# Optimization experiments

Hardware: AMD Instinct MI355X
Metric: run time of the kernel (lower is better)

## Reference

```python
import jax, jax.numpy as jnp
import numpy as np

N = 100000   # nodes
E = 1600000  # edges
IN = 32      # input_dim == num_concepts
H = 128      # h_dim == num_concepts * dim_per_concept
C = 32       # num_concepts
D = 4        # dim_per_concept
G = 32       # g_dim of per-concept MLPs
LAMBDAV = 1e-3


def _spmm(edge_src, edge_dst, edge_val, x):
    # sparse adjacency matmul: out[d] = sum_{edges e: dst(e)=d} val(e) * x[src(e)]
    return jax.ops.segment_sum(edge_val[:, None] * x[edge_src], edge_dst, num_segments=N)


def setup_inputs() -> dict:
    key = jax.random.key(0)
    ks = jax.random.split(key, 20)
    s = lambda shape: 1.0 / np.sqrt(shape[-1] if len(shape) > 1 else 1)
    inp = {
        'X': jax.random.normal(ks[0], (N, IN), jnp.float32),
        'label': jax.random.uniform(ks[1], (N, C), jnp.float32),
        'edge_val': jax.random.uniform(ks[2], (E,), jnp.float32),
        'noise': jax.random.normal(ks[3], (N, C, D), jnp.float32),
        'W_base': jax.random.normal(ks[4], (IN, H), jnp.float32) / np.sqrt(IN),
        'W_mean': jax.random.normal(ks[5], (H, H), jnp.float32) / np.sqrt(H),
        'W_logstd': jax.random.normal(ks[6], (H, H), jnp.float32) / np.sqrt(H),
        'A': 0.05 * jax.random.normal(ks[7], (C, C), jnp.float32),  # keep I - A^T well-conditioned
        'Wz1': jax.random.normal(ks[8], (C, D, G), jnp.float32) / np.sqrt(D),
        'bz1': jax.random.normal(ks[9], (C, G), jnp.float32) * 0.01,
        'Wz2': jax.random.normal(ks[10], (C, G, D), jnp.float32) / np.sqrt(G),
        'bz2': jax.random.normal(ks[11], (C, D), jnp.float32) * 0.01,
        'Wl1': jax.random.normal(ks[12], (C, 1, G), jnp.float32),
        'bl1': jax.random.normal(ks[13], (C, G), jnp.float32) * 0.01,
        'Wl2': jax.random.normal(ks[14], (C, G, 1), jnp.float32) / np.sqrt(G),
        'bl2': jax.random.normal(ks[15], (C, 1), jnp.float32) * 0.01,
        'Wrec': jax.random.normal(ks[16], (H, IN), jnp.float32) / np.sqrt(H),
        'brec': jax.random.normal(ks[17], (IN,), jnp.float32) * 0.01,
        'edge_src': jax.random.randint(ks[18], (E,), 0, N),
        'edge_dst': jax.random.randint(ks[19], (E,), 0, N),
    }
    return inp


def reference(X, label, edge_val, noise, W_base, W_mean, W_logstd, A,
              Wz1, bz1, Wz2, bz2, Wl1, bl1, Wl2, bl2, Wrec, brec,
              edge_src, edge_dst):
    # ---- sparse GCN encoder (x branch): GraphConvSparse = act(spmm(adj, x @ W)) ----
    hidden = jax.nn.relu(_spmm(edge_src, edge_dst, edge_val, X @ W_base))   # [N, H]
    e_m = _spmm(edge_src, edge_dst, edge_val, hidden @ W_mean)              # [N, H]
    _ = _spmm(edge_src, edge_dst, edge_val, hidden @ W_logstd)              # computed then discarded (e_v := ones) in source
    e_m = e_m.reshape(N, C, D)                                              # [N, C, D]

    # ---- CausalDAG: z = (I - A^T)^{-1} epsilon along the concept axis ----
    I = jnp.eye(C, dtype=X.dtype)
    Cmat = jnp.linalg.inv(I - A.T)                                          # [C, C]
    z_m = jnp.einsum('ck,nkd->ncd', Cmat, e_m)                              # [N, C, D]

    # mask: A^T @ x along concept axis
    masked_z_m = jnp.einsum('ck,nkd->ncd', A.T, z_m)                        # [N, C, D]
    masked_label = jnp.einsum('ck,nk->nc', A.T, label)[..., None]           # [N, C, 1]

    # g_z: per-concept MLP Linear(D,G)-ELU-Linear(G,D), weights stacked over concepts
    hz = jax.nn.elu(jnp.einsum('ncd,cdg->ncg', masked_z_m, Wz1) + bz1[None])
    masked_z_m = jnp.einsum('ncg,cgd->ncd', hz, Wz2) + bz2[None]            # [N, C, D]

    # g_label: per-concept MLP Linear(1,G)-ELU-Linear(G,1)
    hl = jax.nn.elu(jnp.einsum('nce,ceg->ncg', masked_label, Wl1) + bl1[None])
    pred_label = (jnp.einsum('ncg,cge->nce', hl, Wl2) + bl2[None])[..., 0]  # [N, C]

    # conditional_sample_gaussian with v = e_v * lambdav, e_v = ones
    z = masked_z_m + jnp.sqrt(jnp.asarray(LAMBDAV, X.dtype)) * noise        # [N, C, D]

    # pred_x / reconst_X head
    rec_x = z.reshape(N, H) @ Wrec + brec                                   # [N, IN]
    return rec_x, pred_label
```

## Files before the change

kernel.cpp:

```cpp
#include <hip/hip_runtime.h>
#include <hip/hip_bf16.h>

#define N_NODES 100000
#define N_EDGES 1600000
#define NBUCK   391

static __device__ __forceinline__ float us2f(unsigned short u) {
    union { unsigned int i; float f; } cv; cv.i = ((unsigned int)u) << 16; return cv.f;
}
static __device__ __forceinline__ unsigned short f2us(float f) {
    __hip_bfloat16 b = __float2bfloat16(f);
    union { __hip_bfloat16 b; unsigned short u; } cv; cv.b = b; return cv.u;
}
static __device__ __forceinline__ float elu_fast(float v) {
    return v > 0.f ? v : (__expf(v) - 1.0f);
}

__global__ __launch_bounds__(64) void k_inv(const float* __restrict__ A,
                                            float* __restrict__ MmT) {
    __shared__ float Af[1024];
    __shared__ float aug[32 * 65];
    __shared__ float fac[32];
    __shared__ float pv_s;
    int t = threadIdx.x;
    for (int i = t; i < 1024; i += 64) Af[i] = A[i];
    __syncthreads();
    for (int i = t; i < 2048; i += 64) {
        int r = i >> 6, c = i & 63;
        float v;
        if (c < 32) v = (r == c ? 1.0f : 0.0f) - Af[c * 32 + r];
        else        v = ((c - 32) == r ? 1.0f : 0.0f);
        aug[r * 65 + c] = v;
    }
    __syncthreads();
    for (int k = 0; k < 32; ++k) {
        if (t == 0) pv_s = 1.0f / aug[k * 65 + k];
        __syncthreads();
        aug[k * 65 + t] *= pv_s;
        __syncthreads();
        if (t < 32) fac[t] = aug[t * 65 + k];
        __syncthreads();
        #pragma unroll 4
        for (int i = t; i < 2048; i += 64) {
            int r = i >> 6, c = i & 63;
            if (r != k) aug[r * 65 + c] -= fac[r] * aug[k * 65 + c];
        }
        __syncthreads();
    }
    for (int i = t; i < 1024; i += 64) {
        int j = i >> 5, c = i & 31;
        float s = 0.f;
        #pragma unroll
        for (int k = 0; k < 32; ++k) s += Af[k * 32 + c] * aug[k * 65 + 32 + j];
        MmT[i] = s;
    }
}

__global__ __launch_bounds__(256) void k_fold(const float* __restrict__ MmT,
                                              const float* __restrict__ Wm,
                                              float* __restrict__ Wcomb) {
    __shared__ float MmTs[1024];
    int tid = threadIdx.x;
    for (int i = tid; i < 1024; i += 256) MmTs[i] = MmT[i];
    __syncthreads();
    int o = blockIdx.x * 256 + tid;
    int h = o >> 5, c = o & 31;
    float4 s = {0.f, 0.f, 0.f, 0.f};
    #pragma unroll
    for (int j = 0; j < 32; ++j) {
        float m = MmTs[j * 32 + c];
        float4 w = ((const float4*)Wm)[h * 32 + j];
        s.x += m * w.x; s.y += m * w.y; s.z += m * w.z; s.w += m * w.w;
    }
    ((float4*)Wcomb)[o] = s;
}

__global__ __launch_bounds__(256) void k_hist(const int* __restrict__ edst,
                                              unsigned int* __restrict__ deg) {
    int e = blockIdx.x * 256 + threadIdx.x;
    atomicAdd(&deg[edst[e]], 1u);
}

__global__ __launch_bounds__(256) void k_scanA(const unsigned int* __restrict__ deg,
                                               unsigned int* __restrict__ row_start,
                                               unsigned int* __restrict__ blk_sums) {
    __shared__ unsigned int sums[256];
    int tid = threadIdx.x;
    int gid = blockIdx.x * 256 + tid;
    uint4 d = ((const uint4*)deg)[gid];
    unsigned int p1 = d.x, p2 = d.x + d.y, p3 = p2 + d.z;
    unsigned int tsum = p3 + d.w;
    sums[tid] = tsum;
    __syncthreads();
    for (int off = 1; off < 256; off <<= 1) {
        unsigned int v = (tid >= off) ? sums[tid - off] : 0u;
        __syncthreads();
        sums[tid] += v;
        __syncthreads();
    }
    unsigned int excl = sums[tid] - tsum;
    int eb = gid * 4;
    if (eb + 0 < N_NODES) row_start[eb + 0] = excl;
    if (eb + 1 < N_NODES) row_start[eb + 1] = excl + p1;
    if (eb + 2 < N_NODES) row_start[eb + 2] = excl + p2;
    if (eb + 3 < N_NODES) row_start[eb + 3] = excl + p3;
    if (tid == 255) blk_sums[blockIdx.x] = sums[255];
}

__global__ __launch_bounds__(128) void k_scanB(unsigned int* __restrict__ blk_sums) {
    __shared__ unsigned int s[128];
    int tid = threadIdx.x;
    unsigned int v = (tid < 98) ? blk_sums[tid] : 0u;
    s[tid] = v;
    __syncthreads();
    for (int off = 1; off < 128; off <<= 1) {
        unsigned int x = (tid >= off) ? s[tid - off] : 0u;
        __syncthreads();
        s[tid] += x;
        __syncthreads();
    }
    if (tid < 98) blk_sums[tid] = s[tid] - v;
}

__global__ __launch_bounds__(256) void k_scanC(unsigned int* __restrict__ row_start,
                                               unsigned int* __restrict__ cursor,
                                               const unsigned int* __restrict__ blk_sums) {
    int tid = threadIdx.x;
    unsigned int off = blk_sums[blockIdx.x];
    int eb = (blockIdx.x * 256 + tid) * 4;
    #pragma unroll
    for (int k = 0; k < 4; ++k) {
        int idx = eb + k;
        if (idx < N_NODES) {
            unsigned int u = row_start[idx] + off;
            row_start[idx] = u;
            cursor[idx] = u;
        }
    }
    if (blockIdx.x == 0 && tid == 0) row_start[N_NODES] = N_EDGES;
}

__global__ __launch_bounds__(256) void k_binit(const unsigned int* __restrict__ row_start,
                                               unsigned int* __restrict__ bucket_cursor) {
    int b = blockIdx.x * 256 + threadIdx.x;
    if (b < NBUCK) bucket_cursor[b] = row_start[b << 8];
}

__global__ __launch_bounds__(256) void k_bucket1(const int* __restrict__ esrc,
                                                 const int* __restrict__ edst,
                                                 const float* __restrict__ evalv,
                                                 unsigned int* __restrict__ bucket_cursor,
                                                 uint2* __restrict__ coarse,
                                                 unsigned char* __restrict__ coarse_dl) {
    __shared__ unsigned int hist[NBUCK];
    __shared__ unsigned int gbase[NBUCK];
    __shared__ unsigned int lcnt[NBUCK];
    int tid = threadIdx.x;
    int e0 = blockIdx.x * 8192;
    for (int i = tid; i < NBUCK; i += 256) { hist[i] = 0u; lcnt[i] = 0u; }
    __syncthreads();
    #pragma unroll 4
    for (int k = 0; k < 32; ++k) {
        int e = e0 + k * 256 + tid;
        if (e < N_EDGES) atomicAdd(&hist[((unsigned)edst[e]) >> 8], 1u);
    }
    __syncthreads();
    for (int b = tid; b < NBUCK; b += 256) {
        unsigned int h = hist[b];
        gbase[b] = h ? atomicAdd(&bucket_cursor[b], h) : 0u;
    }
    __syncthreads();
    #pragma unroll 4
    for (int k = 0; k < 32; ++k) {
        int e = e0 + k * 256 + tid;
        if (e < N_EDGES) {
            unsigned int d = (unsigned)edst[e];
            unsigned int b = d >> 8;
            unsigned int r = atomicAdd(&lcnt[b], 1u);
            unsigned int p = gbase[b] + r;
            uint2 ev;
            ev.x = (unsigned int)esrc[e];
            ev.y = __float_as_uint(evalv[e]);
            coarse[p] = ev;
            coarse_dl[p] = (unsigned char)(d & 255u);
        }
    }
}

__global__ __launch_bounds__(256) void k_bucket2(const unsigned int* __restrict__ row_start,
                                                 const uint2* __restrict__ coarse,
                                                 const unsigned char* __restrict__ coarse_dl,
                                                 unsigned int* __restrict__ cursor,
                                                 uint2* __restrict__ edge_sorted) {
    int b = blockIdx.x;
    unsigned int bs = row_start[b << 8];
    unsigned int be = (b == NBUCK - 1) ? N_EDGES : row_start[(b + 1) << 8];
    unsigned int nbase = (unsigned)b << 8;
    for (unsigned int i = bs + threadIdx.x; i < be; i += 256) {
        uint2 ev = coarse[i];
        unsigned int d = nbase | (unsigned int)coarse_dl[i];
        unsigned int p = atomicAdd(&cursor[d], 1u);
        edge_sorted[p] = ev;
    }
}

__global__ __launch_bounds__(256) void k_gather1(const unsigned int* __restrict__ row_start,
                                                 const uint2* __restrict__ edge_sorted,
                                                 const float* __restrict__ X,
                                                 float* __restrict__ S1) {
    int lane = threadIdx.x & 31;
    int n = blockIdx.x * 8 + (threadIdx.x >> 5);
    unsigned int i = row_start[n], e = row_start[n + 1];
    float a0 = 0.f, a1 = 0.f, a2 = 0.f, a3 = 0.f;
    for (; i + 4 <= e; i += 4) {
        uint2 ea = edge_sorted[i + 0], eb = edge_sorted[i + 1];
        uint2 ec = edge_sorted[i + 2], ed = edge_sorted[i + 3];
        float xa = X[(size_t)ea.x * 32 + lane];
        float xb = X[(size_t)eb.x * 32 + lane];
        float xc = X[(size_t)ec.x * 32 + lane];
        float xd = X[(size_t)ed.x * 32 + lane];
        a0 += __uint_as_float(ea.y) * xa;
        a1 += __uint_as_float(eb.y) * xb;
        a2 += __uint_as_float(ec.y) * xc;
        a3 += __uint_as_float(ed.y) * xd;
    }
    for (; i < e; ++i) {
        uint2 ea = edge_sorted[i];
        a0 += __uint_as_float(ea.y) * X[(size_t)ea.x * 32 + lane];
    }
    S1[(size_t)n * 32 + lane] = (a0 + a1) + (a2 + a3);
}

__global__ __launch_bounds__(256) void k_gemm1(const float* __restrict__ S1,
                                               const float* __restrict__ Wb,
                                               unsigned short* __restrict__ hidden) {
    __shared__ float Wb_s[4096];
    __shared__ float S1s[32 * 36];
    int tid = threadIdx.x;
    int n0 = blockIdx.x * 32;
    for (int i = tid; i < 1024; i += 256)
        ((float4*)Wb_s)[i] = ((const float4*)Wb)[i];
    {
        int r = tid >> 3, cq = tid & 7;
        *(float4*)&S1s[r * 36 + cq * 4] = *(const float4*)&S1[(size_t)(n0 + r) * 32 + cq * 4];
    }
    __syncthreads();
    int q = (tid & 31) * 4;
    int r0 = tid >> 5;
    float4 acc[4];
    #pragma unroll
    for (int i = 0; i < 4; ++i) acc[i] = make_float4(0.f, 0.f, 0.f, 0.f);
    for (int k4 = 0; k4 < 32; k4 += 4) {
        float4 s[4];
        #pragma unroll
        for (int i = 0; i < 4; ++i) s[i] = *(const float4*)&S1s[(r0 + i * 8) * 36 + k4];
        #pragma unroll
        for (int kk = 0; kk < 4; ++kk) {
            float4 w = *(const float4*)&Wb_s[(k4 + kk) * 128 + q];
            #pragma unroll
            for (int i = 0; i < 4; ++i) {
                float v = (&s[i].x)[kk];
                acc[i].x += v * w.x; acc[i].y += v * w.y;
                acc[i].z += v * w.z; acc[i].w += v * w.w;
            }
        }
    }
    #pragma unroll
    for (int i = 0; i < 4; ++i) {
        ushort4 o;
        o.x = f2us(fmaxf(acc[i].x, 0.f)); o.y = f2us(fmaxf(acc[i].y, 0.f));
        o.z = f2us(fmaxf(acc[i].z, 0.f)); o.w = f2us(fmaxf(acc[i].w, 0.f));
        *(ushort4*)&hidden[(size_t)(n0 + r0 + i * 8) * 128 + q] = o;
    }
}

__global__ __launch_bounds__(256) void k_gather2(const unsigned int* __restrict__ row_start,
                                                 const uint2* __restrict__ edge_sorted,
                                                 const unsigned short* __restrict__ hidden,
                                                 unsigned short* __restrict__ S2) {
    int lane = threadIdx.x & 31;
    int n = blockIdx.x * 8 + (threadIdx.x >> 5);
    unsigned int i = row_start[n], e = row_start[n + 1];
    float4 A0 = {0, 0, 0, 0}, A1 = {0, 0, 0, 0}, A2 = {0, 0, 0, 0}, A3 = {0, 0, 0, 0};
    for (; i + 4 <= e; i += 4) {
        uint2 ea = edge_sorted[i + 0], eb = edge_sorted[i + 1];
        uint2 ec = edge_sorted[i + 2], ed = edge_sorted[i + 3];
        ushort4 ha = *(const ushort4*)&hidden[(size_t)ea.x * 128 + lane * 4];
        ushort4 hb = *(const ushort4*)&hidden[(size_t)eb.x * 128 + lane * 4];
        ushort4 hc = *(const ushort4*)&hidden[(size_t)ec.x * 128 + lane * 4];
        ushort4 hd = *(const ushort4*)&hidden[(size_t)ed.x * 128 + lane * 4];
        float va = __uint_as_float(ea.y), vb = __uint_as_float(eb.y);
        float vc = __uint_as_float(ec.y), vd = __uint_as_float(ed.y);
        A0.x += va * us2f(ha.x); A0.y += va * us2f(ha.y); A0.z += va * us2f(ha.z); A0.w += va * us2f(ha.w);
        A1.x += vb * us2f(hb.x); A1.y += vb * us2f(hb.y); A1.z += vb * us2f(hb.z); A1.w += vb * us2f(hb.w);
        A2.x += vc * us2f(hc.x); A2.y += vc * us2f(hc.y); A2.z += vc * us2f(hc.z); A2.w += vc * us2f(hc.w);
        A3.x += vd * us2f(hd.x); A3.y += vd * us2f(hd.y); A3.z += vd * us2f(hd.z); A3.w += vd * us2f(hd.w);
    }
    for (; i < e; ++i) {
        uint2 ea = edge_sorted[i];
        float v = __uint_as_float(ea.y);
        ushort4 h = *(const ushort4*)&hidden[(size_t)ea.x * 128 + lane * 4];
        A0.x += v * us2f(h.x); A0.y += v * us2f(h.y); A0.z += v * us2f(h.z); A0.w += v * us2f(h.w);
    }
    float4 acc;
    acc.x = (A0.x + A1.x) + (A2.x + A3.x);
    acc.y = (A0.y + A1.y) + (A2.y + A3.y);
    acc.z = (A0.z + A1.z) + (A2.z + A3.z);
    acc.w = (A0.w + A1.w) + (A2.w + A3.w);
    ushort4 o;
    o.x = f2us(acc.x); o.y = f2us(acc.y); o.z = f2us(acc.z); o.w = f2us(acc.w);
    *(ushort4*)&S2[(size_t)n * 128 + lane * 4] = o;
}

__global__ __launch_bounds__(256) void k_gemm2(const unsigned short* __restrict__ S2,
                                               const float* __restrict__ Wc,
                                               unsigned short* __restrict__ mt4) {
    __shared__ float Wc_s[128 * 64];
    __shared__ float S2s[32 * 132];
    __shared__ unsigned short Tt[64 * 40];
    int tid = threadIdx.x;
    int rb = blockIdx.x >> 1;
    int j0 = (blockIdx.x & 1) * 64;
    int n0 = rb * 32;
    for (int idx = tid; idx < 2048; idx += 256) {
        int k = idx >> 4, jq = idx & 15;
        *(float4*)&Wc_s[k * 64 + jq * 4] = *(const float4*)&Wc[k * 128 + j0 + jq * 4];
    }
    for (int idx = tid; idx < 1024; idx += 256) {
        int r = idx >> 5, kq = idx & 31;
        ushort4 h = *(const ushort4*)&S2[(size_t)(n0 + r) * 128 + kq * 4];
        float4 f = {us2f(h.x), us2f(h.y), us2f(h.z), us2f(h.w)};
        *(float4*)&S2s[r * 132 + kq * 4] = f;
    }
    __syncthreads();
    int q = (tid & 15) * 4;
    int r0 = tid >> 4;
    float4 a0 = {0, 0, 0, 0}, a1 = {0, 0, 0, 0};
    for (int k4 = 0; k4 < 128; k4 += 4) {
        float4 s0 = *(const float4*)&S2s[r0 * 132 + k4];
        float4 s1 = *(const float4*)&S2s[(r0 + 16) * 132 + k4];
        #pragma unroll
        for (int kk = 0; kk < 4; ++kk) {
            float v0 = (&s0.x)[kk];
            float v1 = (&s1.x)[kk];
            float4 w = *(const float4*)&Wc_s[(k4 + kk) * 64 + q];
            a0.x += v0 * w.x; a0.y += v0 * w.y; a0.z += v0 * w.z; a0.w += v0 * w.w;
            a1.x += v1 * w.x; a1.y += v1 * w.y; a1.z += v1 * w.z; a1.w += v1 * w.w;
        }
    }
    #pragma unroll
    for (int c = 0; c < 4; ++c) {
        Tt[(q + c) * 40 + r0]      = f2us((&a0.x)[c]);
        Tt[(q + c) * 40 + r0 + 16] = f2us((&a1.x)[c]);
    }
    __syncthreads();
    int cc = tid >> 4;
    int r  = (tid & 15) * 2;
    int cg = (j0 >> 2) + cc;
    #pragma unroll
    for (int rr = 0; rr < 2; ++rr) {
        ushort4 o;
        o.x = Tt[(cc * 4 + 0) * 40 + r + rr];
        o.y = Tt[(cc * 4 + 1) * 40 + r + rr];
        o.z = Tt[(cc * 4 + 2) * 40 + r + rr];
        o.w = Tt[(cc * 4 + 3) * 40 + r + rr];
        *(ushort4*)&mt4[((size_t)cg * N_NODES + n0 + r + rr) * 4] = o;
    }
}

__global__ __launch_bounds__(256) void k_noisew(const float* __restrict__ noise,
                                                const float* __restrict__ Wrec,
                                                const float* __restrict__ brec,
                                                float* __restrict__ noiseW) {
    __shared__ float Wr[4096];
    __shared__ float Ns[64 * 132];
    __shared__ float brs[32];
    int tid = threadIdx.x;
    int n0 = blockIdx.x * 64;
    const float SQ = 0.03162277660168379f;
    for (int i = tid; i < 1024; i += 256)
        ((float4*)Wr)[i] = ((const float4*)Wrec)[i];
    if (tid < 32) brs[tid] = brec[tid];
    for (int i = tid; i < 1024; i += 256) {
        int row = i >> 4, u8 = i & 15;
        int n = n0 + row;
        float4 f0, f1;
        if (n < N_NODES) {
            f0 = ((const float4*)(noise + (size_t)n * 128))[u8 * 2];
            f1 = ((const float4*)(noise + (size_t)n * 128))[u8 * 2 + 1];
        } else {
            f0 = make_float4(0.f, 0.f, 0.f, 0.f);
            f1 = f0;
        }
        *(float4*)&Ns[row * 132 + u8 * 8]     = make_float4(SQ * f0.x, SQ * f0.y, SQ * f0.z, SQ * f0.w);
        *(float4*)&Ns[row * 132 + u8 * 8 + 4] = make_float4(SQ * f1.x, SQ * f1.y, SQ * f1.z, SQ * f1.w);
    }
    __syncthreads();
    int r = tid >> 2, q = (tid & 3) * 8;
    float4 acc0 = {0, 0, 0, 0}, acc1 = {0, 0, 0, 0};
    for (int k = 0; k < 128; ++k) {
        float nv = Ns[r * 132 + k];
        float4 w0 = *(const float4*)&Wr[k * 32 + q];
        float4 w1 = *(const float4*)&Wr[k * 32 + q + 4];
        acc0.x += nv * w0.x; acc0.y += nv * w0.y; acc0.z += nv * w0.z; acc0.w += nv * w0.w;
        acc1.x += nv * w1.x; acc1.y += nv * w1.y; acc1.z += nv * w1.z; acc1.w += nv * w1.w;
    }
    int n = n0 + r;
    if (n < N_NODES) {
        acc0.x += brs[q];     acc0.y += brs[q + 1]; acc0.z += brs[q + 2]; acc0.w += brs[q + 3];
        acc1.x += brs[q + 4]; acc1.y += brs[q + 5]; acc1.z += brs[q + 6]; acc1.w += brs[q + 7];
        ((float4*)(noiseW + (size_t)n * 32 + q))[0] = acc0;
        ((float4*)(noiseW + (size_t)n * 32 + q + 4))[0] = acc1;
    }
}

__global__ __launch_bounds__(512) void k_nodez(const unsigned short* __restrict__ mt4,
                                               const float* __restrict__ Wz1,
                                               const float* __restrict__ bz1,
                                               const float* __restrict__ Wz2,
                                               const float* __restrict__ bz2,
                                               const float* __restrict__ Wrec,
                                               const float* __restrict__ noiseW,
                                               float* __restrict__ out) {
    __shared__ float scr[3 * 128 * 34];
    int tid = threadIdx.x;
    int lt  = tid & 127;
    int qq  = tid >> 7;
    int c0  = __builtin_amdgcn_readfirstlane(qq * 8);
    int n = blockIdx.x * 128 + lt;
    bool ok = n < N_NODES;
    int m = ok ? n : (N_NODES - 1);

    const float4* W1 = (const float4*)Wz1;
    const float4* B1 = (const float4*)bz1;
    const float4* W2 = (const float4*)Wz2;
    const float4* B2 = (const float4*)bz2;
    const float4* WR = (const float4*)Wrec;

    float4 o0 = {0,0,0,0}, o1 = {0,0,0,0}, o2 = {0,0,0,0}, o3 = {0,0,0,0};
    float4 o4v = {0,0,0,0}, o5 = {0,0,0,0}, o6 = {0,0,0,0}, o7 = {0,0,0,0};

    ushort4 mz = *(const ushort4*)&mt4[((size_t)c0 * N_NODES + m) * 4];

    for (int cc = 0; cc < 8; ++cc) {
        int c = c0 + cc;
        int cn = (cc < 7) ? (c + 1) : c;
        ushort4 nmz = *(const ushort4*)&mt4[((size_t)cn * N_NODES + m) * 4];
        float a0 = us2f(mz.x), a1 = us2f(mz.y), a2 = us2f(mz.z), a3 = us2f(mz.w);

        float4 zb = B2[c];
        float4 z = zb;
        #pragma unroll
        for (int g4 = 0; g4 < 8; ++g4) {
            float4 w0 = W1[c * 32 + g4];
            float4 w1 = W1[c * 32 + 8 + g4];
            float4 w2 = W1[c * 32 + 16 + g4];
            float4 w3 = W1[c * 32 + 24 + g4];
            float4 bb = B1[c * 8 + g4];
            float4 v;
            v.x = bb.x + a0 * w0.x + a1 * w1.x + a2 * w2.x + a3 * w3.x;
            v.y = bb.y + a0 * w0.y + a1 * w1.y + a2 * w2.y + a3 * w3.y;
            v.z = bb.z + a0 * w0.z + a1 * w1.z + a2 * w2.z + a3 * w3.z;
            v.w = bb.w + a0 * w0.w + a1 * w1.w + a2 * w2.w + a3 * w3.w;
            v.x = elu_fast(v.x); v.y = elu_fast(v.y); v.z = elu_fast(v.z); v.w = elu_fast(v.w);
            float4 u0 = W2[c * 32 + g4 * 4 + 0];
            float4 u1 = W2[c * 32 + g4 * 4 + 1];
            float4 u2 = W2[c * 32 + g4 * 4 + 2];
            float4 u3 = W2[c * 32 + g4 * 4 + 3];
            z.x += v.x * u0.x + v.y * u1.x + v.z * u2.x + v.w * u3.x;
            z.y += v.x * u0.y + v.y * u1.y + v.z * u2.y + v.w * u3.y;
            z.z += v.x * u0.z + v.y * u1.z + v.z * u2.z + v.w * u3.z;
            z.w += v.x * u0.w + v.y * u1.w + v.z * u2.w + v.w * u3.w;
        }
        #pragma unroll
        for (int d = 0; d < 4; ++d) {
            float zv = (&z.x)[d];
            const float4* wr = &WR[(c * 4 + d) * 8];
            float4 r0 = wr[0], r1 = wr[1], r2 = wr[2], r3 = wr[3];
            float4 r4 = wr[4], r5 = wr[5], r6 = wr[6], r7 = wr[7];
            o0.x += zv * r0.x; o0.y += zv * r0.y; o0.z += zv * r0.z; o0.w += zv * r0.w;
            o1.x += zv * r1.x; o1.y += zv * r1.y; o1.z += zv * r1.z; o1.w += zv * r1.w;
            o2.x += zv * r2.x; o2.y += zv * r2.y; o2.z += zv * r2.z; o2.w += zv * r2.w;
            o3.x += zv * r3.x; o3.y += zv * r3.y; o3.z += zv * r3.z; o3.w += zv * r3.w;
            o4v.x += zv * r4.x; o4v.y += zv * r4.y; o4v.z += zv * r4.z; o4v.w += zv * r4.w;
            o5.x += zv * r5.x; o5.y += zv * r5.y; o5.z += zv * r5.z; o5.w += zv * r5.w;
            o6.x += zv * r6.x; o6.y += zv * r6.y; o6.z += zv * r6.z; o6.w += zv * r6.w;
            o7.x += zv * r7.x; o7.y += zv * r7.y; o7.z += zv * r7.z; o7.w += zv * r7.w;
        }
        mz = nmz;
    }

    __syncthreads();
    if (qq != 0) {
        float* p = &scr[((qq - 1) * 128 + lt) * 34];
        *(float2*)&p[0]  = make_float2(o0.x, o0.y);  *(float2*)&p[2]  = make_float2(o0.z, o0.w);
        *(float2*)&p[4]  = make_float2(o1.x, o1.y);  *(float2*)&p[6]  = make_float2(o1.z, o1.w);
        *(float2*)&p[8]  = make_float2(o2.x, o2.y);  *(float2*)&p[10] = make_float2(o2.z, o2.w);
        *(float2*)&p[12] = make_float2(o3.x, o3.y);  *(float2*)&p[14] = make_float2(o3.z, o3.w);
        *(float2*)&p[16] = make_float2(o4v.x, o4v.y); *(float2*)&p[18] = make_float2(o4v.z, o4v.w);
        *(float2*)&p[20] = make_float2(o5.x, o5.y);  *(float2*)&p[22] = make_float2(o5.z, o5.w);
        *(float2*)&p[24] = make_float2(o6.x, o6.y);  *(float2*)&p[26] = make_float2(o6.z, o6.w);
        *(float2*)&p[28] = make_float2(o7.x, o7.y);  *(float2*)&p[30] = make_float2(o7.z, o7.w);
    }
    __syncthreads();
    if (qq == 0 && ok) {
        const float* pA = &scr[lt * 34];
        const float* pB = &scr[(128 + lt) * 34];
        const float* pC = &scr[(256 + lt) * 34];
        const float4* nw = (const float4*)(noiseW + (size_t)n * 32);
        float4* po = (float4*)(out + (size_t)n * 32);
        float4 w, t;
        w = nw[0];
        t.x = o0.x + pA[0] + pB[0] + pC[0] + w.x;   t.y = o0.y + pA[1] + pB[1] + pC[1] + w.y;
        t.z = o0.z + pA[2] + pB[2] + pC[2] + w.z;   t.w = o0.w + pA[3] + pB[3] + pC[3] + w.w;
        po[0] = t;
        w = nw[1];
        t.x = o1.x + pA[4] + pB[4] + pC[4] + w.x;   t.y = o1.y + pA[5] + pB[5] + pC[5] + w.y;
        t.z = o1.z + pA[6] + pB[6] + pC[6] + w.z;   t.w = o1.w + pA[7] + pB[7] + pC[7] + w.w;
        po[1] = t;
        w = nw[2];
        t.x = o2.x + pA[8] + pB[8] + pC[8] + w.x;   t.y = o2.y + pA[9] + pB[9] + pC[9] + w.y;
        t.z = o2.z + pA[10] + pB[10] + pC[10] + w.z; t.w = o2.w + pA[11] + pB[11] + pC[11] + w.w;
        po[2] = t;
        w = nw[3];
        t.x = o3.x + pA[12] + pB[12] + pC[12] + w.x; t.y = o3.y + pA[13] + pB[13] + pC[13] + w.y;
        t.z = o3.z + pA[14] + pB[14] + pC[14] + w.z; t.w = o3.w + pA[15] + pB[15] + pC[15] + w.w;
        po[3] = t;
        w = nw[4];
        t.x = o4v.x + pA[16] + pB[16] + pC[16] + w.x; t.y = o4v.y + pA[17] + pB[17] + pC[17] + w.y;
        t.z = o4v.z + pA[18] + pB[18] + pC[18] + w.z; t.w = o4v.w + pA[19] + pB[19] + pC[19] + w.w;
        po[4] = t;
        w = nw[5];
        t.x = o5.x + pA[20] + pB[20] + pC[20] + w.x; t.y = o5.y + pA[21] + pB[21] + pC[21] + w.y;
        t.z = o5.z + pA[22] + pB[22] + pC[22] + w.z; t.w = o5.w + pA[23] + pB[23] + pC[23] + w.w;
        po[5] = t;
        w = nw[6];
        t.x = o6.x + pA[24] + pB[24] + pC[24] + w.x; t.y = o6.y + pA[25] + pB[25] + pC[25] + w.y;
        t.z = o6.z + pA[26] + pB[26] + pC[26] + w.z; t.w = o6.w + pA[27] + pB[27] + pC[27] + w.w;
        po[6] = t;
        w = nw[7];
        t.x = o7.x + pA[28] + pB[28] + pC[28] + w.x; t.y = o7.y + pA[29] + pB[29] + pC[29] + w.y;
        t.z = o7.z + pA[30] + pB[30] + pC[30] + w.z; t.w = o7.w + pA[31] + pB[31] + pC[31] + w.w;
        po[7] = t;
    }
}

__global__ __launch_bounds__(256) void k_label(const float* __restrict__ label,
                                               const float* __restrict__ A,
                                               const float* __restrict__ Wl1,
                                               const float* __restrict__ bl1,
                                               const float* __restrict__ Wl2,
                                               const float* __restrict__ bl2,
                                               float* __restrict__ out) {
    __shared__ float As[1024], Wl1s[1024], bl1s[1024], Wl2s[1024], bl2s[32];
    int tid = threadIdx.x;
    for (int i = tid; i < 1024; i += 256) {
        As[i] = A[i];
        Wl1s[i] = Wl1[i];
        bl1s[i] = bl1[i];
        Wl2s[i] = Wl2[i];
    }
    if (tid < 32) bl2s[tid] = bl2[tid];
    __syncthreads();

    int n = blockIdx.x * 256 + tid;
    bool ok = n < N_NODES;
    int nn = ok ? n : (N_NODES - 1);

    float lab[32];
    #pragma unroll
    for (int q = 0; q < 8; ++q) {
        float4 lv = ((const float4*)(label + (size_t)nn * 32))[q];
        lab[q * 4 + 0] = lv.x; lab[q * 4 + 1] = lv.y;
        lab[q * 4 + 2] = lv.z; lab[q * 4 + 3] = lv.w;
    }
    float pred[32];
    for (int c = 0; c < 32; ++c) {
        float ml = 0.f;
        #pragma unroll
        for (int k = 0; k < 32; ++k) ml += As[k * 32 + c] * lab[k];
        float p = bl2s[c];
        #pragma unroll
        for (int g = 0; g < 32; ++g) {
            float h = elu_fast(ml * Wl1s[c * 32 + g] + bl1s[c * 32 + g]);
            p += h * Wl2s[c * 32 + g];
        }
        pred[c] = p;
    }
    if (ok) {
        #pragma unroll
        for (int q = 0; q < 8; ++q) {
            float4 v = {pred[q * 4 + 0], pred[q * 4 + 1], pred[q * 4 + 2], pred[q * 4 + 3]};
            ((float4*)(out + (size_t)N_NODES * 32 + (size_t)n * 32))[q] = v;
        }
    }
}

extern "C" void kernel_launch(void* const* d_in, const int* in_sizes, int n_in,
                              void* d_out, int out_size, void* d_ws, size_t ws_size,
                              hipStream_t stream) {
    const float* X      = (const float*)d_in[0];
    const float* label  = (const float*)d_in[1];
    const float* evalv  = (const float*)d_in[2];
    const float* noise  = (const float*)d_in[3];
    const float* W_base = (const float*)d_in[4];
    const float* W_mean = (const float*)d_in[5];
    const float* A      = (const float*)d_in[7];
    const float* Wz1    = (const float*)d_in[8];
    const float* bz1    = (const float*)d_in[9];
    const float* Wz2    = (const float*)d_in[10];
    const float* bz2    = (const float*)d_in[11];
    const float* Wl1    = (const float*)d_in[12];
    const float* bl1    = (const float*)d_in[13];
    const float* Wl2    = (const float*)d_in[14];
    const float* bl2    = (const float*)d_in[15];
    const float* Wrec   = (const float*)d_in[16];
    const float* brec   = (const float*)d_in[17];
    const int* esrc = (const int*)d_in[18];
    const int* edst = (const int*)d_in[19];
    float* out = (float*)d_out;

    char* ws = (char*)d_ws;
    float*          Wcomb       = (float*)(ws);
    float*          MmT         = (float*)(ws + 65536);
    unsigned int*   blk_sums    = (unsigned int*)(ws + 69632);
    unsigned int*   deg         = (unsigned int*)(ws + 70656);
    unsigned int*   bucket_cursor = (unsigned int*)(ws + 70656);
    unsigned int*   row_start   = (unsigned int*)(ws + 472064);
    unsigned int*   cursor      = (unsigned int*)(ws + 873984);
    uint2*          edge_sorted = (uint2*)(ws + 1273984);
    uint2*          coarse      = (uint2*)(ws + 14073984);
    unsigned char*  coarse_dl   = (unsigned char*)(ws + 26873984);
    unsigned short* hidden      = (unsigned short*)(ws + 14073984);
    unsigned short* mt4         = (unsigned short*)(ws + 14073984);
    float*          S1          = (float*)(ws + 39673984);
    unsigned short* S2          = (unsigned short*)(ws + 39673984);
    float*          noiseW      = (float*)(ws + 39673984);

    hipMemsetAsync(deg, 0, 100352 * sizeof(unsigned int), stream);
    k_inv<<<1, 64, 0, stream>>>(A, MmT);
    k_fold<<<16, 256, 0, stream>>>(MmT, W_mean, Wcomb);
    k_hist<<<N_EDGES / 256, 256, 0, stream>>>(edst, deg);
    k_scanA<<<98, 256, 0, stream>>>(deg, row_start, blk_sums);
    k_scanB<<<1, 128, 0, stream>>>(blk_sums);
    k_scanC<<<98, 256, 0, stream>>>(row_start, cursor, blk_sums);
    k_binit<<<2, 256, 0, stream>>>(row_start, bucket_cursor);
    k_bucket1<<<(N_EDGES + 8191) / 8192, 256, 0, stream>>>(esrc, edst, evalv,
                                                           bucket_cursor, coarse, coarse_dl);
    k_bucket2<<<NBUCK, 256, 0, stream>>>(row_start, coarse, coarse_dl, cursor, edge_sorted);
    k_gather1<<<N_NODES / 8, 256, 0, stream>>>(row_start, edge_sorted, X, S1);
    k_gemm1<<<N_NODES / 32, 256, 0, stream>>>(S1, W_base, hidden);
    k_gather2<<<N_NODES / 8, 256, 0, stream>>>(row_start, edge_sorted, hidden, S2);
    k_gemm2<<<(N_NODES / 32) * 2, 256, 0, stream>>>(S2, Wcomb, mt4);
    k_noisew<<<(N_NODES + 63) / 64, 256, 0, stream>>>(noise, Wrec, brec, noiseW);
    k_nodez<<<(N_NODES + 127) / 128, 512, 0, stream>>>(mt4,
                                                       Wz1, bz1, Wz2, bz2,
                                                       Wrec, noiseW, out);
    k_label<<<(N_NODES + 255) / 256, 256, 0, stream>>>(label, A, Wl1, bl1, Wl2, bl2, out);
}
```

Before: 744.0 us.

## Process two nodes per thread in k_nodez and pack per-concept weights

Restructures k_nodez so each thread handles two adjacent nodes across 4 concepts, with 8 concept groups per block, and reuses each weight load for both nodes. A new k_pack kernel lays out Wz1, bz1, Wz2, bz2 and Wrec contiguously per concept, giving a uniform base pointer. The cross-group reduction now uses shared-memory atomicAdd into a zeroed buffer instead of staged partial sums. This raises register pressure (64 float4 accumulators) and adds LDS atomic contention, and node-pair reads depend on an interleaved bf16 layout of mt4.

```diff
diff --git a/kernel.cpp b/kernel.cpp
--- a/kernel.cpp
+++ b/kernel.cpp
@@ -73,6 +73,24 @@
         s.x += m * w.x; s.y += m * w.y; s.z += m * w.z; s.w += m * w.w;
     }
     ((float4*)Wcomb)[o] = s;
+}
+
+__global__ __launch_bounds__(256) void k_pack(const float* __restrict__ Wz1,
+                                              const float* __restrict__ bz1,
+                                              const float* __restrict__ Wz2,
+                                              const float* __restrict__ bz2,
+                                              const float* __restrict__ Wrec,
+                                              float* __restrict__ pk) {
+    int i = blockIdx.x * 256 + threadIdx.x;
+    if (i >= 32 * 448) return;
+    int c = i / 448, off = i % 448;
+    float v = 0.f;
+    if (off < 128)      v = Wz1[c * 128 + off];
+    else if (off < 160) v = bz1[c * 32 + (off - 128)];
+    else if (off < 288) v = Wz2[c * 128 + (off - 160)];
+    else if (off < 292) v = bz2[c * 4 + (off - 288)];
+    else if (off < 420) v = Wrec[(c * 4 + (off - 292) / 32) * 32 + ((off - 292) & 31)];
+    pk[i] = v;
 }
 
 __global__ __launch_bounds__(256) void k_hist(const int* __restrict__ edst,
@@ -415,133 +433,116 @@
 }
 
 __global__ __launch_bounds__(512) void k_nodez(const unsigned short* __restrict__ mt4,
-                                               const float* __restrict__ Wz1,
-                                               const float* __restrict__ bz1,
-                                               const float* __restrict__ Wz2,
-                                               const float* __restrict__ bz2,
-                                               const float* __restrict__ Wrec,
+                                               const float* __restrict__ pk,
                                                const float* __restrict__ noiseW,
                                                float* __restrict__ out) {
-    __shared__ float scr[3 * 128 * 34];
-    int tid = threadIdx.x;
-    int lt  = tid & 127;
-    int qq  = tid >> 7;
-    int c0  = __builtin_amdgcn_readfirstlane(qq * 8);
-    int n = blockIdx.x * 128 + lt;
-    bool ok = n < N_NODES;
-    int m = ok ? n : (N_NODES - 1);
-
-    const float4* W1 = (const float4*)Wz1;
-    const float4* B1 = (const float4*)bz1;
-    const float4* W2 = (const float4*)Wz2;
-    const float4* B2 = (const float4*)bz2;
-    const float4* WR = (const float4*)Wrec;
-
-    float4 o0 = {0,0,0,0}, o1 = {0,0,0,0}, o2 = {0,0,0,0}, o3 = {0,0,0,0};
-    float4 o4v = {0,0,0,0}, o5 = {0,0,0,0}, o6 = {0,0,0,0}, o7 = {0,0,0,0};
-
-    ushort4 mz = *(const ushort4*)&mt4[((size_t)c0 * N_NODES + m) * 4];
-
-    for (int cc = 0; cc < 8; ++cc) {
+    __shared__ float scr[128 * 33];
+    int tid = threadIdx.x;
+    for (int i = tid; i < 128 * 33; i += 512) scr[i] = 0.f;
+    __syncthreads();
+
+    int sl = tid & 63;
+    int cg = tid >> 6;
+    int c0 = __builtin_amdgcn_readfirstlane(cg * 4);
+    int nl0 = sl * 2;
+    int n0 = blockIdx.x * 128 + nl0;
+    int me = (n0 + 1 < N_NODES) ? n0 : (N_NODES - 2);
+
+    float4 oA[8], oB[8];
+    #pragma unroll
+    for (int j = 0; j < 8; ++j) {
+        oA[j] = make_float4(0.f, 0.f, 0.f, 0.f);
+        oB[j] = make_float4(0.f, 0.f, 0.f, 0.f);
+    }
+
+    uint4 mz = *(const uint4*)&mt4[((size_t)c0 * N_NODES + me) * 4];
+
+    for (int cc = 0; cc < 4; ++cc) {
         int c = c0 + cc;
-        int cn = (cc < 7) ? (c + 1) : c;
-        ushort4 nmz = *(const ushort4*)&mt4[((size_t)cn * N_NODES + m) * 4];
-        float a0 = us2f(mz.x), a1 = us2f(mz.y), a2 = us2f(mz.z), a3 = us2f(mz.w);
-
-        float4 zb = B2[c];
-        float4 z = zb;
+        int cn = (cc < 3) ? (c + 1) : c;
+        uint4 nmz = *(const uint4*)&mt4[((size_t)cn * N_NODES + me) * 4];
+
+        float a0 = us2f((unsigned short)(mz.x & 0xffffu)), a1 = us2f((unsigned short)(mz.x >> 16));
+        float a2 = us2f((unsigned short)(mz.y & 0xffffu)), a3 = us2f((unsigned short)(mz.y >> 16));
+        float b0 = us2f((unsigned short)(mz.z & 0xffffu)), b1 = us2f((unsigned short)(mz.z >> 16));
+        float b2 = us2f((unsigned short)(mz.w & 0xffffu)), b3 = us2f((unsigned short)(mz.w >> 16));
+
+        const float4* P = (const float4*)pk + c * 112;
+        float4 zA = P[72];
+        float4 zB = zA;
         #pragma unroll
         for (int g4 = 0; g4 < 8; ++g4) {
-            float4 w0 = W1[c * 32 + g4];
-            float4 w1 = W1[c * 32 + 8 + g4];
-            float4 w2 = W1[c * 32 + 16 + g4];
-            float4 w3 = W1[c * 32 + 24 + g4];
-            float4 bb = B1[c * 8 + g4];
-            float4 v;
-            v.x = bb.x + a0 * w0.x + a1 * w1.x + a2 * w2.x + a3 * w3.x;
-            v.y = bb.y + a0 * w0.y + a1 * w1.y + a2 * w2.y + a3 * w3.y;
-            v.z = bb.z + a0 * w0.z + a1 * w1.z + a2 * w2.z + a3 * w3.z;
-            v.w = bb.w + a0 * w0.w + a1 * w1.w + a2 * w2.w + a3 * w3.w;
-            v.x = elu_fast(v.x); v.y = elu_fast(v.y); v.z = elu_fast(v.z); v.w = elu_fast(v.w);
-            float4 u0 = W2[c * 32 + g4 * 4 + 0];
-            float4 u1 = W2[c * 32 + g4 * 4 + 1];
-            float4 u2 = W2[c * 32 + g4 * 4 + 2];
-            float4 u3 = W2[c * 32 + g4 * 4 + 3];
-            z.x += v.x * u0.x + v.y * u1.x + v.z * u2.x + v.w * u3.x;
-            z.y += v.x * u0.y + v.y * u1.y + v.z * u2.y + v.w * u3.y;
-            z.z += v.x * u0.z + v.y * u1.z + v.z * u2.z + v.w * u3.z;
-            z.w += v.x * u0.w + v.y * u1.w + v.z * u2.w + v.w * u3.w;
+            float4 w0 = P[g4];
+            float4 w1 = P[8 + g4];
+            float4 w2 = P[16 + g4];
+            float4 w3 = P[24 + g4];
+            float4 bb = P[32 + g4];
+            float4 vA, vB;
+            vA.x = bb.x + a0 * w0.x + a1 * w1.x + a2 * w2.x + a3 * w3.x;
+            vA.y = bb.y + a0 * w0.y + a1 * w1.y + a2 * w2.y + a3 * w3.y;
+            vA.z = bb.z + a0 * w0.z + a1 * w1.z + a2 * w2.z + a3 * w3.z;
+            vA.w = bb.w + a0 * w0.w + a1 * w1.w + a2 * w2.w + a3 * w3.w;
+            vB.x = bb.x + b0 * w0.x + b1 * w1.x + b2 * w2.x + b3 * w3.x;
+            vB.y = bb.y + b0 * w0.y + b1 * w1.y + b2 * w2.y + b3 * w3.y;
+            vB.z = bb.z + b0 * w0.z + b1 * w1.z + b2 * w2.z + b3 * w3.z;
+            vB.w = bb.w + b0 * w0.w + b1 * w1.w + b2 * w2.w + b3 * w3.w;
+            vA.x = elu_fast(vA.x); vA.y = elu_fast(vA.y); vA.z = elu_fast(vA.z); vA.w = elu_fast(vA.w);
+            vB.x = elu_fast(vB.x); vB.y = elu_fast(vB.y); vB.z = elu_fast(vB.z); vB.w = elu_fast(vB.w);
+            float4 u0 = P[40 + g4 * 4 + 0];
+            float4 u1 = P[40 + g4 * 4 + 1];
+            float4 u2 = P[40 + g4 * 4 + 2];
+            float4 u3 = P[40 + g4 * 4 + 3];
+            zA.x += vA.x * u0.x + vA.y * u1.x + vA.z * u2.x + vA.w * u3.x;
+            zA.y += vA.x * u0.y + vA.y * u1.y + vA.z * u2.y + vA.w * u3.y;
+            zA.z += vA.x * u0.z + vA.y * u1.z + vA.z * u2.z + vA.w * u3.z;
+            zA.w += vA.x * u0.w + vA.y * u1.w + vA.z * u2.w + vA.w * u3.w;
+            zB.x += vB.x * u0.x + vB.y * u1.x + vB.z * u2.x + vB.w * u3.x;
+            zB.y += vB.x * u0.y + vB.y * u1.y + vB.z * u2.y + vB.w * u3.y;
+            zB.z += vB.x * u0.z + vB.y * u1.z + vB.z * u2.z + vB.w * u3.z;
+            zB.w += vB.x * u0.w + vB.y * u1.w + vB.z * u2.w + vB.w * u3.w;
         }
         #pragma unroll
         for (int d = 0; d < 4; ++d) {
-            float zv = (&z.x)[d];
-            const float4* wr = &WR[(c * 4 + d) * 8];
-            float4 r0 = wr[0], r1 = wr[1], r2 = wr[2], r3 = wr[3];
-            float4 r4 = wr[4], r5 = wr[5], r6 = wr[6], r7 = wr[7];
-            o0.x += zv * r0.x; o0.y += zv * r0.y; o0.z += zv * r0.z; o0.w += zv * r0.w;
-            o1.x += zv * r1.x; o1.y += zv * r1.y; o1.z += zv * r1.z; o1.w += zv * r1.w;
-            o2.x += zv * r2.x; o2.y += zv * r2.y; o2.z += zv * r2.z; o2.w += zv * r2.w;
-            o3.x += zv * r3.x; o3.y += zv * r3.y; o3.z += zv * r3.z; o3.w += zv * r3.w;
-            o4v.x += zv * r4.x; o4v.y += zv * r4.y; o4v.z += zv * r4.z; o4v.w += zv * r4.w;
-            o5.x += zv * r5.x; o5.y += zv * r5.y; o5.z += zv * r5.z; o5.w += zv * r5.w;
-            o6.x += zv * r6.x; o6.y += zv * r6.y; o6.z += zv * r6.z; o6.w += zv * r6.w;
-            o7.x += zv * r7.x; o7.y += zv * r7.y; o7.z += zv * r7.z; o7.w += zv * r7.w;
+            float zvA = (&zA.x)[d];
+            float zvB = (&zB.x)[d];
+            const float4* wr = P + 73 + d * 8;
+            #pragma unroll
+            for (int j = 0; j < 8; ++j) {
+                float4 r = wr[j];
+                oA[j].x += zvA * r.x; oA[j].y += zvA * r.y; oA[j].z += zvA * r.z; oA[j].w += zvA * r.w;
+                oB[j].x += zvB * r.x; oB[j].y += zvB * r.y; oB[j].z += zvB * r.z; oB[j].w += zvB * r.w;
+            }
         }
         mz = nmz;
     }
 
-    __syncthreads();
-    if (qq != 0) {
-        float* p = &scr[((qq - 1) * 128 + lt) * 34];
-        *(float2*)&p[0]  = make_float2(o0.x, o0.y);  *(float2*)&p[2]  = make_float2(o0.z, o0.w);
-        *(float2*)&p[4]  = make_float2(o1.x, o1.y);  *(float2*)&p[6]  = make_float2(o1.z, o1.w);
-        *(float2*)&p[8]  = make_float2(o2.x, o2.y);  *(float2*)&p[10] = make_float2(o2.z, o2.w);
-        *(float2*)&p[12] = make_float2(o3.x, o3.y);  *(float2*)&p[14] = make_float2(o3.z, o3.w);
-        *(float2*)&p[16] = make_float2(o4v.x, o4v.y); *(float2*)&p[18] = make_float2(o4v.z, o4v.w);
-        *(float2*)&p[20] = make_float2(o5.x, o5.y);  *(float2*)&p[22] = make_float2(o5.z, o5.w);
-        *(float2*)&p[24] = make_float2(o6.x, o6.y);  *(float2*)&p[26] = make_float2(o6.z, o6.w);
-        *(float2*)&p[28] = make_float2(o7.x, o7.y);  *(float2*)&p[30] = make_float2(o7.z, o7.w);
-    }
-    __syncthreads();
-    if (qq == 0 && ok) {
-        const float* pA = &scr[lt * 34];
-        const float* pB = &scr[(128 + lt) * 34];
-        const float* pC = &scr[(256 + lt) * 34];
-        const float4* nw = (const float4*)(noiseW + (size_t)n * 32);
-        float4* po = (float4*)(out + (size_t)n * 32);
-        float4 w, t;
-        w = nw[0];
-        t.x = o0.x + pA[0] + pB[0] + pC[0] + w.x;   t.y = o0.y + pA[1] + pB[1] + pC[1] + w.y;
-        t.z = o0.z + pA[2] + pB[2] + pC[2] + w.z;   t.w = o0.w + pA[3] + pB[3] + pC[3] + w.w;
-        po[0] = t;
-        w = nw[1];
-        t.x = o1.x + pA[4] + pB[4] + pC[4] + w.x;   t.y = o1.y + pA[5] + pB[5] + pC[5] + w.y;
-        t.z = o1.z + pA[6] + pB[6] + pC[6] + w.z;   t.w = o1.w + pA[7] + pB[7] + pC[7] + w.w;
-        po[1] = t;
-        w = nw[2];
-        t.x = o2.x + pA[8] + pB[8] + pC[8] + w.x;   t.y = o2.y + pA[9] + pB[9] + pC[9] + w.y;
-        t.z = o2.z + pA[10] + pB[10] + pC[10] + w.z; t.w = o2.w + pA[11] + pB[11] + pC[11] + w.w;
-        po[2] = t;
-        w = nw[3];
-        t.x = o3.x + pA[12] + pB[12] + pC[12] + w.x; t.y = o3.y + pA[13] + pB[13] + pC[13] + w.y;
-        t.z = o3.z + pA[14] + pB[14] + pC[14] + w.z; t.w = o3.w + pA[15] + pB[15] + pC[15] + w.w;
-        po[3] = t;
-        w = nw[4];
-        t.x = o4v.x + pA[16] + pB[16] + pC[16] + w.x; t.y = o4v.y + pA[17] + pB[17] + pC[17] + w.y;
-        t.z = o4v.z + pA[18] + pB[18] + pC[18] + w.z; t.w = o4v.w + pA[19] + pB[19] + pC[19] + w.w;
-        po[4] = t;
-        w = nw[5];
-        t.x = o5.x + pA[20] + pB[20] + pC[20] + w.x; t.y = o5.y + pA[21] + pB[21] + pC[21] + w.y;
-        t.z = o5.z + pA[22] + pB[22] + pC[22] + w.z; t.w = o5.w + pA[23] + pB[23] + pC[23] + w.w;
-        po[5] = t;
-        w = nw[6];
-        t.x = o6.x + pA[24] + pB[24] + pC[24] + w.x; t.y = o6.y + pA[25] + pB[25] + pC[25] + w.y;
-        t.z = o6.z + pA[26] + pB[26] + pC[26] + w.z; t.w = o6.w + pA[27] + pB[27] + pC[27] + w.w;
-        po[6] = t;
-        w = nw[7];
-        t.x = o7.x + pA[28] + pB[28] + pC[28] + w.x; t.y = o7.y + pA[29] + pB[29] + pC[29] + w.y;
-        t.z = o7.z + pA[30] + pB[30] + pC[30] + w.z; t.w = o7.w + pA[31] + pB[31] + pC[31] + w.w;
-        po[7] = t;
+    float* pa = &scr[nl0 * 33];
+    float* pb = &scr[(nl0 + 1) * 33];
+    #pragma unroll
+    for (int j = 0; j < 8; ++j) {
+        atomicAdd(&pa[j * 4 + 0], oA[j].x); atomicAdd(&pa[j * 4 + 1], oA[j].y);
+        atomicAdd(&pa[j * 4 + 2], oA[j].z); atomicAdd(&pa[j * 4 + 3], oA[j].w);
+        atomicAdd(&pb[j * 4 + 0], oB[j].x); atomicAdd(&pb[j * 4 + 1], oB[j].y);
+        atomicAdd(&pb[j * 4 + 2], oB[j].z); atomicAdd(&pb[j * 4 + 3], oB[j].w);
+    }
+    __syncthreads();
+
+    if (tid < 256) {
+        int node = tid >> 1, seg = tid & 1;
+        int n = blockIdx.x * 128 + node;
+        if (n < N_NODES) {
+            const float* p = &scr[node * 33 + seg * 16];
+            const float4* nw = (const float4*)(noiseW + (size_t)n * 32 + seg * 16);
+            float4* po = (float4*)(out + (size_t)n * 32 + seg * 16);
+            #pragma unroll
+            for (int q = 0; q < 4; ++q) {
+                float4 w = nw[q];
+                float4 t;
+                t.x = p[q * 4 + 0] + w.x; t.y = p[q * 4 + 1] + w.y;
+                t.z = p[q * 4 + 2] + w.z; t.w = p[q * 4 + 3] + w.w;
+                po[q] = t;
+            }
+        }
     }
 }
 
@@ -636,9 +637,11 @@
     float*          S1          = (float*)(ws + 39673984);
     unsigned short* S2          = (unsigned short*)(ws + 39673984);
     float*          noiseW      = (float*)(ws + 39673984);
+    float*          pk          = (float*)(ws + 65273984);
 
     hipMemsetAsync(deg, 0, 100352 * sizeof(unsigned int), stream);
     k_inv<<<1, 64, 0, stream>>>(A, MmT);
+    k_pack<<<56, 256, 0, stream>>>(Wz1, bz1, Wz2, bz2, Wrec, pk);
     k_fold<<<16, 256, 0, stream>>>(MmT, W_mean, Wcomb);
     k_hist<<<N_EDGES / 256, 256, 0, stream>>>(edst, deg);
     k_scanA<<<98, 256, 0, stream>>>(deg, row_start, blk_sums);
@@ -653,8 +656,6 @@
     k_gather2<<<N_NODES / 8, 256, 0, stream>>>(row_start, edge_sorted, hidden, S2);
     k_gemm2<<<(N_NODES / 32) * 2, 256, 0, stream>>>(S2, Wcomb, mt4);
     k_noisew<<<(N_NODES + 63) / 64, 256, 0, stream>>>(noise, Wrec, brec, noiseW);
-    k_nodez<<<(N_NODES + 127) / 128, 512, 0, stream>>>(mt4,
-                                                       Wz1, bz1, Wz2, bz2,
-                                                       Wrec, noiseW, out);
+    k_nodez<<<(N_NODES + 127) / 128, 512, 0, stream>>>(mt4, pk, noiseW, out);
     k_label<<<(N_NODES + 255) / 256, 256, 0, stream>>>(label, A, Wl1, bl1, Wl2, bl2, out);
 }
```

Measured after the change: 890.4 us. 19.7% more time.
